# Performance work log

Measured on AMD Instinct MI355X. Metric: run time of the kernel, lower is better.

## Reference

```python
import jax, jax.numpy as jnp
import numpy as np

B, T_NEW, D_MODEL, H, DH = 8, 512, 1024, 16, 64
CACHED = 2048
T_TOTAL = CACHED + T_NEW  # static padded total length (last batch item is full)


def setup_inputs() -> dict:
    key = jax.random.key(0)
    ks = jax.random.split(key, 16)
    x_new = jax.random.normal(ks[0], (B, T_NEW, D_MODEL), jnp.float32)
    past_lengths = jax.random.randint(ks[1], (B,), CACHED // 2, CACHED)
    past_lengths = past_lengths.at[-1].set(CACHED).astype(jnp.int32)
    new_counts = jax.random.randint(ks[2], (B,), 1, T_NEW)
    new_counts = new_counts.at[-1].set(T_NEW).astype(jnp.int32)
    # prefix (left-aligned) valid mask for new tokens, matching how the torch
    # module compacts k_new[b, :, :count] into the cache
    valid_new_mask = jnp.arange(T_NEW)[None, :] < new_counts[:, None]
    total_lengths = past_lengths + new_counts
    key_padding_mask = jnp.arange(T_TOTAL)[None, :] < total_lengths[:, None]
    inv_freq = 1.0 / (10000.0 ** (jnp.arange(0, DH, 2, dtype=jnp.float32) / DH))
    pm = (jnp.arange(CACHED)[None, :] < past_lengths[:, None])[:, None, :, None]
    past_k = jax.random.normal(ks[3], (B, H, CACHED, DH), jnp.float32) * pm
    past_v = jax.random.normal(ks[4], (B, H, CACHED, DH), jnp.float32) * pm
    s = 0.02
    Wq = jax.random.normal(ks[5], (D_MODEL, D_MODEL), jnp.float32) * s
    Wk = jax.random.normal(ks[6], (D_MODEL, D_MODEL), jnp.float32) * s
    Wv = jax.random.normal(ks[7], (D_MODEL, D_MODEL), jnp.float32) * s
    Wo = jax.random.normal(ks[8], (D_MODEL, D_MODEL), jnp.float32) * s
    bq = jnp.zeros((D_MODEL,), jnp.float32)
    bk = jnp.zeros((D_MODEL,), jnp.float32)
    bv = jnp.zeros((D_MODEL,), jnp.float32)
    bo = jnp.zeros((D_MODEL,), jnp.float32)
    return {
        'x_new': x_new, 'inv_freq': inv_freq, 'past_k': past_k, 'past_v': past_v,
        'Wq': Wq, 'bq': bq, 'Wk': Wk, 'bk': bk, 'Wv': Wv, 'bv': bv, 'Wo': Wo, 'bo': bo,
        'key_padding_mask': key_padding_mask, 'past_lengths': past_lengths,
        'valid_new_mask': valid_new_mask,
    }


def _rotate_half(x):
    h = x.shape[-1] // 2
    return jnp.concatenate([-x[..., h:], x[..., :h]], axis=-1)


def reference(x_new, inv_freq, past_k, past_v, Wq, bq, Wk, bk, Wv, bv, Wo, bo,
              key_padding_mask, past_lengths, valid_new_mask):
    Bb, Tn, _ = x_new.shape
    # projections -> [B, H, T_new, DH]
    q = (x_new @ Wq.T + bq).reshape(Bb, Tn, H, DH).transpose(0, 2, 1, 3)
    k_new = (x_new @ Wk.T + bk).reshape(Bb, Tn, H, DH).transpose(0, 2, 1, 3)
    v_new = (x_new @ Wv.T + bv).reshape(Bb, Tn, H, DH).transpose(0, 2, 1, 3)
    # RoPE at absolute positions past_len + step (invalid -> 0)
    steps = jnp.arange(Tn)
    positions = jnp.where(valid_new_mask, past_lengths[:, None] + steps[None, :], 0)
    freqs = positions[..., None].astype(jnp.float32) * inv_freq  # [B, T, DH/2]
    emb = jnp.concatenate([freqs, freqs], axis=-1)
    cos = jnp.cos(emb)[:, None].astype(q.dtype)  # [B, 1, T, DH]
    sin = jnp.sin(emb)[:, None].astype(q.dtype)
    q = q * cos + _rotate_half(q) * sin
    k_new = k_new * cos + _rotate_half(k_new) * sin
    vm = valid_new_mask[:, None, :, None].astype(q.dtype)
    q = q * vm
    k_new = k_new * vm
    v_new = v_new * vm
    # zero cached entries past each item's cached length (matches padded cache)
    pm = (jnp.arange(CACHED)[None, :] < past_lengths[:, None])[:, None, :, None]
    past_k = past_k * pm.astype(past_k.dtype)
    past_v = past_v * pm.astype(past_v.dtype)
    # ragged append: scatter new tokens at [past_len, past_len+count); invalid
    # tokens dumped into an extra slot T_TOTAL that is sliced off
    pos_idx = jnp.where(valid_new_mask, past_lengths[:, None] + steps[None, :], T_TOTAL)
    pad = lambda p: jnp.pad(p, ((0, 0), (0, 0), (0, T_TOTAL + 1 - CACHED), (0, 0)))
    scat = jax.vmap(lambda base, new, idx: base.at[:, idx, :].add(new))
    k_total = scat(pad(past_k), k_new, pos_idx)[:, :, :T_TOTAL]
    v_total = scat(pad(past_v), v_new, pos_idx)[:, :, :T_TOTAL]
    # padded SDPA with key-padding mask
    scores = jnp.einsum('bhqd,bhkd->bhqk', q, k_total) / jnp.sqrt(jnp.asarray(DH, q.dtype))
    scores = jnp.where(key_padding_mask[:, None, None, :], scores, jnp.finfo(scores.dtype).min)
    attn = jax.nn.softmax(scores, axis=-1)
    ctx = jnp.einsum('bhqk,bhkd->bhqd', attn, v_total)
    ctx = ctx.transpose(0, 2, 1, 3).reshape(Bb, Tn, D_MODEL)
    out = (ctx @ Wo.T + bo) * valid_new_mask[..., None].astype(ctx.dtype)
    total_lengths = past_lengths + valid_new_mask.sum(axis=1).astype(past_lengths.dtype)
    return out, k_total, v_total, total_lengths
```

## Files before the change

kernel.cpp:

```cpp
#include <hip/hip_runtime.h>
#include <math.h>

#define B_ 8
#define TN 512
#define DM 1024
#define H_ 16
#define DH 64
#define CACHED_ 2048
#define TT 2560

#define QSC 0.18033688011112042f

typedef __attribute__((ext_vector_type(8))) short bf16x8;
typedef __attribute__((ext_vector_type(4))) float f32x4;

union U16x8 { uint4 u; unsigned short s[8]; };
union U16x4 { uint2 u; unsigned short s[4]; };
union F4 { float4 v; float f[4]; };

__device__ __forceinline__ unsigned short f2b(float x) {
    unsigned u = __float_as_uint(x);
    unsigned r = (u + 0x7FFFu + ((u >> 16) & 1u)) >> 16;
    return (unsigned short)r;
}
__device__ __forceinline__ float b2f(unsigned short v) {
    return __uint_as_float((unsigned)v << 16);
}

__device__ __forceinline__ unsigned cvt_pk_bf16(float lo, float hi) {
    unsigned r;
    asm("v_cvt_pk_bf16_f32 %0, %1, %2" : "=v"(r) : "v"(lo), "v"(hi));
    return r;
}

__device__ __forceinline__ void gload16(const void* g, void* l) {
    __builtin_amdgcn_global_load_lds(
        (const __attribute__((address_space(1))) void*)g,
        (__attribute__((address_space(3))) void*)l, 16, 0, 0);
}

__global__ void count_kernel(const unsigned char* __restrict__ vnm,
                             const unsigned char* __restrict__ kpm,
                             const int* __restrict__ past_len,
                             int* __restrict__ counts,
                             float* __restrict__ total_out) {
    int b = blockIdx.x;
    __shared__ int red[256];
    int esz = (kpm[1] | kpm[2] | kpm[3]) ? 1 : 4;
    int s = 0;
    for (int t = threadIdx.x; t < TN; t += 256)
        s += (vnm[(size_t)(b * TN + t) * esz] != 0) ? 1 : 0;
    red[threadIdx.x] = s;
    __syncthreads();
    for (int off = 128; off > 0; off >>= 1) {
        if (threadIdx.x < off) red[threadIdx.x] += red[threadIdx.x + off];
        __syncthreads();
    }
    if (threadIdx.x == 0) {
        counts[b] = red[0];
        total_out[b] = (float)(past_len[b] + red[0]);
    }
}

__global__ void cvt_all(const float* __restrict__ x,
                        const float* __restrict__ Wq,
                        const float* __restrict__ Wk,
                        const float* __restrict__ Wv,
                        const float* __restrict__ Wo,
                        unsigned short* __restrict__ Xbf,
                        unsigned short* __restrict__ Wqkvb,
                        unsigned short* __restrict__ Wob) {
    int i8 = (blockIdx.x * 256 + threadIdx.x) << 3;
    const float* src;
    unsigned short* dst;
    int off;
    if (i8 < (1 << 22)) {
        src = x; off = i8; dst = Xbf + i8;
    } else if (i8 < (1 << 22) + (3 << 20)) {
        int j = i8 - (1 << 22);
        int w = j >> 20;
        src = w == 0 ? Wq : (w == 1 ? Wk : Wv);
        off = j & 0xFFFFF;
        dst = Wqkvb + j;
    } else {
        int j = i8 - ((1 << 22) + (3 << 20));
        src = Wo; off = j; dst = Wob + j;
    }
    float4 a = *(const float4*)(src + off);
    float4 b = *(const float4*)(src + off + 4);
    U16x8 o;
    o.s[0] = f2b(a.x); o.s[1] = f2b(a.y); o.s[2] = f2b(a.z); o.s[3] = f2b(a.w);
    o.s[4] = f2b(b.x); o.s[5] = f2b(b.y); o.s[6] = f2b(b.z); o.s[7] = f2b(b.w);
    *(uint4*)dst = o.u;
}

__device__ __forceinline__ void gemm_core(
    const unsigned short* __restrict__ A, const unsigned short* __restrict__ Bw,
    int K, int m0, int n0, short* As, short* Bs, f32x4 acc[4][4]) {
    const int tid = threadIdx.x;
    const int wave = tid >> 6, lane = tid & 63;
    const int wm = wave >> 1, wn = wave & 1;
    const int l15 = lane & 15, lq = lane >> 4;

    const int srow = wave * 16 + (lane >> 2);
    const int sc = (lane & 3) << 3;
    const unsigned short* Ag0 = A + (size_t)(m0 + srow) * K + sc;
    const unsigned short* Ag1 = A + (size_t)(m0 + 64 + srow) * K + sc;
    const unsigned short* Bg0 = Bw + (size_t)(n0 + srow) * K + sc;
    const unsigned short* Bg1 = Bw + (size_t)(n0 + 64 + srow) * K + sc;
    short* Ad0 = As + wave * 16 * 32;
    short* Ad1 = As + (64 + wave * 16) * 32;
    short* Bd0 = Bs + wave * 16 * 32;
    short* Bd1 = Bs + (64 + wave * 16) * 32;

    for (int k0 = 0; k0 < K; k0 += 32) {
        __syncthreads();
        gload16(Ag0 + k0, Ad0);
        gload16(Ag1 + k0, Ad1);
        gload16(Bg0 + k0, Bd0);
        gload16(Bg1 + k0, Bd1);
        __syncthreads();
        bf16x8 af[4], bf[4];
#pragma unroll
        for (int mi = 0; mi < 4; ++mi)
            af[mi] = *(const bf16x8*)&As[(wm * 64 + mi * 16 + l15) * 32 + lq * 8];
#pragma unroll
        for (int ni = 0; ni < 4; ++ni)
            bf[ni] = *(const bf16x8*)&Bs[(wn * 64 + ni * 16 + l15) * 32 + lq * 8];
#pragma unroll
        for (int mi = 0; mi < 4; ++mi)
#pragma unroll
            for (int ni = 0; ni < 4; ++ni)
                acc[mi][ni] = __builtin_amdgcn_mfma_f32_16x16x32_bf16(
                    af[mi], bf[ni], acc[mi][ni], 0, 0, 0);
    }
}

__global__ __launch_bounds__(256) void gemm_qkv_mfma(
    const unsigned short* __restrict__ Xbf,
    const unsigned short* __restrict__ Wqkv,
    const float* __restrict__ bq, const float* __restrict__ bk,
    const float* __restrict__ bv, const float* __restrict__ inv_freq,
    const int* __restrict__ past_len,
    unsigned short* __restrict__ Qraw, unsigned short* __restrict__ Kraw,
    unsigned short* __restrict__ Vraw) {
    __shared__ __align__(16) short As[128 * 32];
    __shared__ __align__(16) short Bs[128 * 32];
    f32x4 acc[4][4] = {};
    const int m0 = blockIdx.y << 7, n0 = blockIdx.x << 7;
    gemm_core(Xbf, Wqkv, DM, m0, n0, As, Bs, acc);

    const int which = n0 >> 10;
    const int tid = threadIdx.x, wave = tid >> 6, lane = tid & 63;
    const int wm = wave >> 1, wn = wave & 1, l15 = lane & 15, lq = lane >> 4;

    if (which == 0) {
        const int bb = m0 >> 9;
        const int pl = past_len[bb];
        const int hh = (n0 + wn * 64) >> 6;
#pragma unroll
        for (int ni = 0; ni < 2; ++ni) {
            int i = ni * 16 + l15;
            int n1 = n0 + wn * 64 + ni * 16 + l15;
            float fi = inv_freq[i];
            float blo = bq[n1], bhi = bq[n1 + 32];
#pragma unroll
            for (int mi = 0; mi < 4; ++mi) {
#pragma unroll
                for (int r = 0; r < 4; ++r) {
                    int m = m0 + wm * 64 + mi * 16 + lq * 4 + r;
                    int t = m & 511;
                    float ang = (float)(pl + t) * fi;
                    float s, c;
                    __sincosf(ang, &s, &c);
                    float x1 = acc[mi][ni][r] + blo;
                    float x2 = acc[mi][ni + 2][r] + bhi;
                    size_t base = ((size_t)(bb * H_ + hh) * TN + t) * DH;
                    Qraw[base + i]      = f2b((x1 * c - x2 * s) * QSC);
                    Qraw[base + i + 32] = f2b((x2 * c + x1 * s) * QSC);
                }
            }
        }
    } else {
        const float* bias = which == 1 ? bk : bv;
        unsigned short* dst = which == 1 ? Kraw : Vraw;
#pragma unroll
        for (int ni = 0; ni < 4; ++ni) {
            int n1 = (n0 & 1023) + wn * 64 + ni * 16 + l15;
            float bb = bias[n1];
            int h = n1 >> 6, dh = n1 & 63;
#pragma unroll
            for (int mi = 0; mi < 4; ++mi) {
#pragma unroll
                for (int r = 0; r < 4; ++r) {
                    int m = m0 + wm * 64 + mi * 16 + lq * 4 + r;
                    int b = m >> 9, t = m & 511;
                    dst[((size_t)(b * H_ + h) * TN + t) * DH + dh] =
                        f2b(acc[mi][ni][r] + bb);
                }
            }
        }
    }
}

__global__ __launch_bounds__(256) void gemm_out_mfma(
    const unsigned short* __restrict__ Ctxb,
    const unsigned short* __restrict__ Wob,
    const float* __restrict__ bo, const int* __restrict__ counts,
    float* __restrict__ Out) {
    __shared__ __align__(16) short As[128 * 32];
    __shared__ __align__(16) short Bs[128 * 32];
    f32x4 acc[4][4] = {};
    const int m0 = blockIdx.y << 7, n0 = blockIdx.x << 7;
    gemm_core(Ctxb, Wob, DM, m0, n0, As, Bs, acc);

    const int tid = threadIdx.x, wave = tid >> 6, lane = tid & 63;
    const int wm = wave >> 1, wn = wave & 1, l15 = lane & 15, lq = lane >> 4;
    const int cnt = counts[m0 >> 9];
#pragma unroll
    for (int mi = 0; mi < 4; ++mi) {
#pragma unroll
        for (int r = 0; r < 4; ++r) {
            int m = m0 + wm * 64 + mi * 16 + lq * 4 + r;
            int t = m & 511;
            bool valid = t < cnt;
#pragma unroll
            for (int ni = 0; ni < 4; ++ni) {
                int n = n0 + wn * 64 + ni * 16 + l15;
                Out[(size_t)m * DM + n] = valid ? acc[mi][ni][r] + bo[n] : 0.f;
            }
        }
    }
}

__global__ void build_kv(const float* __restrict__ past_k,
                         const float* __restrict__ past_v,
                         const unsigned short* __restrict__ Kraw,
                         const unsigned short* __restrict__ Vraw,
                         const float* __restrict__ inv_freq,
                         const int* __restrict__ past_len,
                         const int* __restrict__ counts,
                         float* __restrict__ Ko, float* __restrict__ Vo,
                         unsigned short* __restrict__ Kb16,
                         unsigned short* __restrict__ Vb16) {
    int idx = blockIdx.x * 256 + threadIdx.x;
    int i = idx & 7;
    int p = idx >> 3;
    int h = blockIdx.y, bz = blockIdx.z;
    int pl = past_len[bz], cnt = counts[bz];
    int dh = i << 2;
    size_t obase = ((size_t)(bz * H_ + h) * TT + p) * DH;
    F4 k1, k2, v1, v2;
    if (p < pl) {
        size_t ib = ((size_t)(bz * H_ + h) * CACHED_ + p) * DH;
        k1.v = *(const float4*)(past_k + ib + dh);
        k2.v = *(const float4*)(past_k + ib + dh + 32);
        v1.v = *(const float4*)(past_v + ib + dh);
        v2.v = *(const float4*)(past_v + ib + dh + 32);
    } else if (p < pl + cnt) {
        int t = p - pl;
        size_t ib = ((size_t)(bz * H_ + h) * TN + t) * DH;
        U16x4 ka, kc, va, vc;
        ka.u = *(const uint2*)(Kraw + ib + dh);
        kc.u = *(const uint2*)(Kraw + ib + dh + 32);
        va.u = *(const uint2*)(Vraw + ib + dh);
        vc.u = *(const uint2*)(Vraw + ib + dh + 32);
#pragma unroll
        for (int j = 0; j < 4; ++j) {
            float ang = (float)p * inv_freq[dh + j];
            float s, c;
            __sincosf(ang, &s, &c);
            float x1 = b2f(ka.s[j]), x2 = b2f(kc.s[j]);
            k1.f[j] = x1 * c - x2 * s;
            k2.f[j] = x2 * c + x1 * s;
            v1.f[j] = b2f(va.s[j]);
            v2.f[j] = b2f(vc.s[j]);
        }
    } else {
        k1.v = k2.v = v1.v = v2.v = make_float4(0.f, 0.f, 0.f, 0.f);
    }
    *(float4*)(Ko + obase + dh) = k1.v;
    *(float4*)(Ko + obase + dh + 32) = k2.v;
    *(float4*)(Vo + obase + dh) = v1.v;
    *(float4*)(Vo + obase + dh + 32) = v2.v;
    U16x4 o;
#pragma unroll
    for (int j = 0; j < 4; ++j) o.s[j] = f2b(k1.f[j]);
    *(uint2*)(Kb16 + obase + dh) = o.u;
#pragma unroll
    for (int j = 0; j < 4; ++j) o.s[j] = f2b(k2.f[j]);
    *(uint2*)(Kb16 + obase + dh + 32) = o.u;
#pragma unroll
    for (int j = 0; j < 4; ++j) o.s[j] = f2b(v1.f[j]);
    *(uint2*)(Vb16 + obase + dh) = o.u;
#pragma unroll
    for (int j = 0; j < 4; ++j) o.s[j] = f2b(v2.f[j]);
    *(uint2*)(Vb16 + obase + dh + 32) = o.u;
}

__global__ __launch_bounds__(256) void attn_mfma(
    const unsigned short* __restrict__ Qbf,
    const unsigned short* __restrict__ Kb,
    const unsigned short* __restrict__ Vb,
    const int* __restrict__ past_len, const int* __restrict__ counts,
    unsigned short* __restrict__ Ctxb) {
    const int j = blockIdx.x;
    const int xcd = j & 7;
    const int tloc = j >> 3;
    const int qt = tloc & 7;
    const int p = ((tloc >> 3) << 3) | xcd;
    const int b = p >> 4, h = p & 15;

    const int tid = threadIdx.x;
    const int wave = tid >> 6, lane = tid & 63;
    const int l15 = lane & 15, lq = lane >> 4;

    __shared__ __align__(16) short Qs[4096];
    __shared__ __align__(16) short Ks[2][4096];
    __shared__ __align__(16) short Vt[4096];
    __shared__ __align__(16) short Pb[4096];

    const size_t qbase = ((size_t)(b * H_ + h) * TN + qt * 64) * DH;
    const size_t kbase = (size_t)(b * H_ + h) * TT * DH;

    const int total = past_len[b] + counts[b];
    const int ntiles = (total + 63) >> 6;

    const int dA = wave * 64 + lane;
    const int dB = 256 + wave * 64 + lane;
    const int krA = (dA >> 7) * 16 + ((dA & 15) ^ ((dA >> 4) & 7));
    const int kcA = ((dA >> 4) & 7) << 3;
    const int krB = (dB >> 7) * 16 + ((dB & 15) ^ ((dB >> 4) & 7));
    const int kcB = ((dB >> 4) & 7) << 3;
    const unsigned short* KgA = Kb + kbase + (size_t)krA * DH + kcA;
    const unsigned short* KgB = Kb + kbase + (size_t)krB * DH + kcB;
    const int kdoffA = (wave * 64) * 8;
    const int kdoffB = (256 + wave * 64) * 8;

    gload16(KgA, &Ks[0][kdoffA]);
    gload16(KgB, &Ks[0][kdoffB]);

    const int kp = tid & 31, dh8 = (tid >> 5) << 3;
    const int kc = kp >> 2, ko2 = (kp & 3) << 1;
    const unsigned short* Vg = Vb + kbase + (size_t)(2 * kp) * DH + dh8;
    uint4 vr0 = *(const uint4*)Vg;
    uint4 vr1 = *(const uint4*)(Vg + DH);

#pragma unroll
    for (int jj = 0; jj < 2; ++jj) {
        int e = tid + (jj << 8);
        int row = e >> 3, c = e & 7;
        *(uint4*)&Qs[(((row >> 4) * 8 + c) * 16 + ((row & 15) ^ c)) * 8] =
            *(const uint4*)(Qbf + qbase + row * 64 + c * 8);
    }
    __syncthreads();
    const int c0 = lq, c1 = 4 + lq;
    bf16x8 qa0 = *(const bf16x8*)&Qs[((wave * 8 + c0) * 16 + (l15 ^ c0)) * 8];
    bf16x8 qa1 = *(const bf16x8*)&Qs[((wave * 8 + c1) * 16 + (l15 ^ c1)) * 8];

    float rsum[4] = {0.f, 0.f, 0.f, 0.f};
    f32x4 O[4] = {};
    unsigned short* Pw = (unsigned short*)(Pb + wave * 1024);
    const int pc0 = l15 >> 3, pwo = l15 & 7;

    int cur = 0;
    for (int kt = 0; kt < ntiles; ++kt) {
        asm volatile("s_waitcnt vmcnt(0)" ::: "memory");
        __builtin_amdgcn_s_barrier();

        {
            U16x8 a, cc;
            a.u = vr0;
            cc.u = vr1;
#pragma unroll
            for (int jj = 0; jj < 8; ++jj) {
                int dh = dh8 + jj;
                unsigned pk = (unsigned)a.s[jj] | ((unsigned)cc.s[jj] << 16);
                *(unsigned*)&Vt[((((dh >> 4) * 8 + kc) * 16) + ((dh & 15) ^ kc)) * 8 + ko2] = pk;
            }
        }
        {
            int ktn = (kt + 1 < ntiles) ? kt + 1 : kt;
            gload16(KgA + (size_t)ktn * 64 * DH, &Ks[cur ^ 1][kdoffA]);
            gload16(KgB + (size_t)ktn * 64 * DH, &Ks[cur ^ 1][kdoffB]);
            vr0 = *(const uint4*)(Vg + (size_t)ktn * 64 * DH);
            vr1 = *(const uint4*)(Vg + (size_t)ktn * 64 * DH + DH);
        }

        asm volatile("s_waitcnt lgkmcnt(0)" ::: "memory");
        __builtin_amdgcn_s_barrier();
        __builtin_amdgcn_sched_barrier(0);

        const short* Kcur = Ks[cur];
        f32x4 S[4];
#pragma unroll
        for (int nt = 0; nt < 4; ++nt) {
            f32x4 acc = {};
            bf16x8 kb0 = *(const bf16x8*)&Kcur[((nt * 8 + c0) * 16 + (l15 ^ c0)) * 8];
            acc = __builtin_amdgcn_mfma_f32_16x16x32_bf16(qa0, kb0, acc, 0, 0, 0);
            bf16x8 kb1 = *(const bf16x8*)&Kcur[((nt * 8 + c1) * 16 + (l15 ^ c1)) * 8];
            acc = __builtin_amdgcn_mfma_f32_16x16x32_bf16(qa1, kb1, acc, 0, 0, 0);
            S[nt] = acc;
        }

        int limit = total - (kt << 6);
        if (limit < 64) {
#pragma unroll
            for (int nt = 0; nt < 4; ++nt) {
                bool ok = nt * 16 + l15 < limit;
#pragma unroll
                for (int r = 0; r < 4; ++r) S[nt][r] = ok ? S[nt][r] : -1e30f;
            }
        }

#pragma unroll
        for (int nt = 0; nt < 4; ++nt) {
            const int pc = nt * 2 + pc0;
#pragma unroll
            for (int rr = 0; rr < 2; ++rr) {
                float p0 = __builtin_amdgcn_exp2f(S[nt][2 * rr]);
                float p1 = __builtin_amdgcn_exp2f(S[nt][2 * rr + 1]);
                rsum[2 * rr] += p0;
                rsum[2 * rr + 1] += p1;
                unsigned pk = cvt_pk_bf16(p0, p1);
                int row0 = lq * 4 + 2 * rr;
                int row1 = row0 + 1;
                Pw[(pc * 16 + (row0 ^ pc)) * 8 + pwo] = (unsigned short)pk;
                Pw[(pc * 16 + (row1 ^ pc)) * 8 + pwo] = (unsigned short)(pk >> 16);
            }
        }
        asm volatile("s_waitcnt lgkmcnt(0)" ::: "memory");

        bf16x8 pa0 = *(const bf16x8*)&Pw[(c0 * 16 + (l15 ^ c0)) * 8];
        bf16x8 pa1 = *(const bf16x8*)&Pw[(c1 * 16 + (l15 ^ c1)) * 8];
#pragma unroll
        for (int nt = 0; nt < 4; ++nt) {
            bf16x8 vb0 = *(const bf16x8*)&Vt[((nt * 8 + c0) * 16 + (l15 ^ c0)) * 8];
            O[nt] = __builtin_amdgcn_mfma_f32_16x16x32_bf16(pa0, vb0, O[nt], 0, 0, 0);
            bf16x8 vb1 = *(const bf16x8*)&Vt[((nt * 8 + c1) * 16 + (l15 ^ c1)) * 8];
            O[nt] = __builtin_amdgcn_mfma_f32_16x16x32_bf16(pa1, vb1, O[nt], 0, 0, 0);
        }
        cur ^= 1;
    }

#pragma unroll
    for (int off = 1; off < 16; off <<= 1)
#pragma unroll
        for (int r = 0; r < 4; ++r) rsum[r] += __shfl_xor(rsum[r], off);

#pragma unroll
    for (int r = 0; r < 4; ++r) {
        float inv = 1.f / rsum[r];
        int t = qt * 64 + wave * 16 + lq * 4 + r;
        size_t mbase = ((size_t)(b * TN + t)) * DM + h * DH;
#pragma unroll
        for (int nt = 0; nt < 4; ++nt)
            Ctxb[mbase + nt * 16 + l15] = f2b(O[nt][r] * inv);
    }
}

extern "C" void kernel_launch(void* const* d_in, const int* in_sizes, int n_in,
                              void* d_out, int out_size, void* d_ws, size_t ws_size,
                              hipStream_t stream) {
    const float* x_new    = (const float*)d_in[0];
    const float* inv_freq = (const float*)d_in[1];
    const float* past_k   = (const float*)d_in[2];
    const float* past_v   = (const float*)d_in[3];
    const float* Wq = (const float*)d_in[4];
    const float* bq = (const float*)d_in[5];
    const float* Wk = (const float*)d_in[6];
    const float* bk = (const float*)d_in[7];
    const float* Wv = (const float*)d_in[8];
    const float* bv = (const float*)d_in[9];
    const float* Wo = (const float*)d_in[10];
    const float* bo = (const float*)d_in[11];
    const unsigned char* kpm = (const unsigned char*)d_in[12];
    const int* past_len      = (const int*)d_in[13];
    const unsigned char* vnm = (const unsigned char*)d_in[14];

    float* out      = (float*)d_out;
    float* k_total  = out + (size_t)B_ * TN * DM;
    float* v_total  = k_total + (size_t)B_ * H_ * TT * DH;
    float* total_out = v_total + (size_t)B_ * H_ * TT * DH;

    const size_t NQ = (size_t)B_ * TN * DM;
    const size_t NKV = (size_t)B_ * H_ * TT * DH;

    int* counts = (int*)d_ws;
    unsigned short* Xbf   = (unsigned short*)((char*)d_ws + 256);
    unsigned short* Wqkvb = Xbf + NQ;
    unsigned short* Wob   = Wqkvb + (size_t)3 * DM * DM;
    unsigned short* Qraw  = Wob + (size_t)DM * DM;
    unsigned short* Kraw  = Qraw + NQ;
    unsigned short* Vraw  = Kraw + NQ;
    unsigned short* Ctxb  = Vraw + NQ;
    unsigned short* Kb16  = Ctxb + NQ;
    unsigned short* Vb16  = Kb16 + NKV;

    count_kernel<<<B_, 256, 0, stream>>>(vnm, kpm, past_len, counts, total_out);
    cvt_all<<<4096, 256, 0, stream>>>(x_new, Wq, Wk, Wv, Wo, Xbf, Wqkvb, Wob);

    gemm_qkv_mfma<<<dim3(24, 32), 256, 0, stream>>>(
        Xbf, Wqkvb, bq, bk, bv, inv_freq, past_len, Qraw, Kraw, Vraw);
    build_kv<<<dim3((TT * 8) / 256, H_, B_), 256, 0, stream>>>(
        past_k, past_v, Kraw, Vraw, inv_freq, past_len, counts,
        k_total, v_total, Kb16, Vb16);
    attn_mfma<<<1024, 256, 0, stream>>>(Qraw, Kb16, Vb16,
                                        past_len, counts, Ctxb);
    gemm_out_mfma<<<dim3(8, 32), 256, 0, stream>>>(Ctxb, Wob, bo, counts, out);
}
```

Before: 527.1 us.

## Double-buffer GEMM LDS tiles and widen attention blocks to 128 queries

The shared GEMM core now double-buffers its A/B LDS tiles, prefetching the next K slice while MFMAs run on the current one, with one barrier per iteration instead of two. The attention kernel moves to 512-thread blocks covering 128 query rows, so each K/V tile loaded into LDS is reused by twice as many waves and the per-thread K/V load work is halved. The cost is more LDS per block, which can lower occupancy. The GEMM prefetch also relies on a single barrier plus a vmcnt wait for correctness.

```diff
diff --git a/kernel.cpp b/kernel.cpp
--- a/kernel.cpp
+++ b/kernel.cpp
@@ -96,7 +96,7 @@
 
 __device__ __forceinline__ void gemm_core(
     const unsigned short* __restrict__ A, const unsigned short* __restrict__ Bw,
-    int K, int m0, int n0, short* As, short* Bs, f32x4 acc[4][4]) {
+    int K, int m0, int n0, short* As2, short* Bs2, f32x4 acc[4][4]) {
     const int tid = threadIdx.x;
     const int wave = tid >> 6, lane = tid & 63;
     const int wm = wave >> 1, wn = wave & 1;
@@ -108,31 +108,43 @@
     const unsigned short* Ag1 = A + (size_t)(m0 + 64 + srow) * K + sc;
     const unsigned short* Bg0 = Bw + (size_t)(n0 + srow) * K + sc;
     const unsigned short* Bg1 = Bw + (size_t)(n0 + 64 + srow) * K + sc;
-    short* Ad0 = As + wave * 16 * 32;
-    short* Ad1 = As + (64 + wave * 16) * 32;
-    short* Bd0 = Bs + wave * 16 * 32;
-    short* Bd1 = Bs + (64 + wave * 16) * 32;
-
+    const int d0 = wave * 512;
+    const int d1 = 2048 + wave * 512;
+
+    gload16(Ag0, As2 + d0);
+    gload16(Ag1, As2 + d1);
+    gload16(Bg0, Bs2 + d0);
+    gload16(Bg1, Bs2 + d1);
+
+    int cur = 0;
     for (int k0 = 0; k0 < K; k0 += 32) {
-        __syncthreads();
-        gload16(Ag0 + k0, Ad0);
-        gload16(Ag1 + k0, Ad1);
-        gload16(Bg0 + k0, Bd0);
-        gload16(Bg1 + k0, Bd1);
-        __syncthreads();
+        asm volatile("s_waitcnt vmcnt(0)" ::: "memory");
+        __builtin_amdgcn_s_barrier();
+
+        int kn = (k0 + 32 < K) ? k0 + 32 : k0;
+        short* An = As2 + ((cur ^ 1) << 12);
+        short* Bn = Bs2 + ((cur ^ 1) << 12);
+        gload16(Ag0 + kn, An + d0);
+        gload16(Ag1 + kn, An + d1);
+        gload16(Bg0 + kn, Bn + d0);
+        gload16(Bg1 + kn, Bn + d1);
+
+        const short* Ac = As2 + (cur << 12);
+        const short* Bc = Bs2 + (cur << 12);
         bf16x8 af[4], bf[4];
 #pragma unroll
         for (int mi = 0; mi < 4; ++mi)
-            af[mi] = *(const bf16x8*)&As[(wm * 64 + mi * 16 + l15) * 32 + lq * 8];
+            af[mi] = *(const bf16x8*)&Ac[(wm * 64 + mi * 16 + l15) * 32 + lq * 8];
 #pragma unroll
         for (int ni = 0; ni < 4; ++ni)
-            bf[ni] = *(const bf16x8*)&Bs[(wn * 64 + ni * 16 + l15) * 32 + lq * 8];
+            bf[ni] = *(const bf16x8*)&Bc[(wn * 64 + ni * 16 + l15) * 32 + lq * 8];
 #pragma unroll
         for (int mi = 0; mi < 4; ++mi)
 #pragma unroll
             for (int ni = 0; ni < 4; ++ni)
                 acc[mi][ni] = __builtin_amdgcn_mfma_f32_16x16x32_bf16(
                     af[mi], bf[ni], acc[mi][ni], 0, 0, 0);
+        cur ^= 1;
     }
 }
 
@@ -144,8 +156,8 @@
     const int* __restrict__ past_len,
     unsigned short* __restrict__ Qraw, unsigned short* __restrict__ Kraw,
     unsigned short* __restrict__ Vraw) {
-    __shared__ __align__(16) short As[128 * 32];
-    __shared__ __align__(16) short Bs[128 * 32];
+    __shared__ __align__(16) short As[2 * 128 * 32];
+    __shared__ __align__(16) short Bs[2 * 128 * 32];
     f32x4 acc[4][4] = {};
     const int m0 = blockIdx.y << 7, n0 = blockIdx.x << 7;
     gemm_core(Xbf, Wqkv, DM, m0, n0, As, Bs, acc);
@@ -208,8 +220,8 @@
     const unsigned short* __restrict__ Wob,
     const float* __restrict__ bo, const int* __restrict__ counts,
     float* __restrict__ Out) {
-    __shared__ __align__(16) short As[128 * 32];
-    __shared__ __align__(16) short Bs[128 * 32];
+    __shared__ __align__(16) short As[2 * 128 * 32];
+    __shared__ __align__(16) short Bs[2 * 128 * 32];
     f32x4 acc[4][4] = {};
     const int m0 = blockIdx.y << 7, n0 = blockIdx.x << 7;
     gemm_core(Ctxb, Wob, DM, m0, n0, As, Bs, acc);
@@ -298,7 +310,7 @@
     *(uint2*)(Vb16 + obase + dh + 32) = o.u;
 }
 
-__global__ __launch_bounds__(256) void attn_mfma(
+__global__ __launch_bounds__(512) void attn_mfma(
     const unsigned short* __restrict__ Qbf,
     const unsigned short* __restrict__ Kb,
     const unsigned short* __restrict__ Vb,
@@ -307,48 +319,43 @@
     const int j = blockIdx.x;
     const int xcd = j & 7;
     const int tloc = j >> 3;
-    const int qt = tloc & 7;
-    const int p = ((tloc >> 3) << 3) | xcd;
+    const int qt = tloc & 3;
+    const int p = ((tloc >> 2) << 3) | xcd;
     const int b = p >> 4, h = p & 15;
 
     const int tid = threadIdx.x;
     const int wave = tid >> 6, lane = tid & 63;
     const int l15 = lane & 15, lq = lane >> 4;
 
-    __shared__ __align__(16) short Qs[4096];
+    __shared__ __align__(16) short Qs[8192];
     __shared__ __align__(16) short Ks[2][4096];
     __shared__ __align__(16) short Vt[4096];
-    __shared__ __align__(16) short Pb[4096];
-
-    const size_t qbase = ((size_t)(b * H_ + h) * TN + qt * 64) * DH;
+    __shared__ __align__(16) short Pb[8192];
+
+    const size_t qbase = ((size_t)(b * H_ + h) * TN + qt * 128) * DH;
     const size_t kbase = (size_t)(b * H_ + h) * TT * DH;
 
     const int total = past_len[b] + counts[b];
     const int ntiles = (total + 63) >> 6;
 
-    const int dA = wave * 64 + lane;
-    const int dB = 256 + wave * 64 + lane;
+    const int dA = tid;
     const int krA = (dA >> 7) * 16 + ((dA & 15) ^ ((dA >> 4) & 7));
     const int kcA = ((dA >> 4) & 7) << 3;
-    const int krB = (dB >> 7) * 16 + ((dB & 15) ^ ((dB >> 4) & 7));
-    const int kcB = ((dB >> 4) & 7) << 3;
     const unsigned short* KgA = Kb + kbase + (size_t)krA * DH + kcA;
-    const unsigned short* KgB = Kb + kbase + (size_t)krB * DH + kcB;
-    const int kdoffA = (wave * 64) * 8;
-    const int kdoffB = (256 + wave * 64) * 8;
+    const int kdoffA = wave * 512;
 
     gload16(KgA, &Ks[0][kdoffA]);
-    gload16(KgB, &Ks[0][kdoffB]);
-
-    const int kp = tid & 31, dh8 = (tid >> 5) << 3;
+
+    const int kp = tid & 31;
+    const int dh4 = (tid >> 5) << 2;
     const int kc = kp >> 2, ko2 = (kp & 3) << 1;
-    const unsigned short* Vg = Vb + kbase + (size_t)(2 * kp) * DH + dh8;
-    uint4 vr0 = *(const uint4*)Vg;
-    uint4 vr1 = *(const uint4*)(Vg + DH);
+    const unsigned short* Vg = Vb + kbase + (size_t)(2 * kp) * DH + dh4;
+    uint2 vr0 = *(const uint2*)Vg;
+    uint2 vr1 = *(const uint2*)(Vg + DH);
 
 #pragma unroll
     for (int jj = 0; jj < 2; ++jj) {
-        int e = tid + (jj << 8);
+        int e = tid + (jj << 9);
         int row = e >> 3, c = e & 7;
         *(uint4*)&Qs[(((row >> 4) * 8 + c) * 16 + ((row & 15) ^ c)) * 8] =
             *(const uint4*)(Qbf + qbase + row * 64 + c * 8);
@@ -369,12 +376,12 @@
         __builtin_amdgcn_s_barrier();
 
         {
-            U16x8 a, cc;
+            U16x4 a, cc;
             a.u = vr0;
             cc.u = vr1;
 #pragma unroll
-            for (int jj = 0; jj < 8; ++jj) {
-                int dh = dh8 + jj;
+            for (int jj = 0; jj < 4; ++jj) {
+                int dh = dh4 + jj;
                 unsigned pk = (unsigned)a.s[jj] | ((unsigned)cc.s[jj] << 16);
                 *(unsigned*)&Vt[((((dh >> 4) * 8 + kc) * 16) + ((dh & 15) ^ kc)) * 8 + ko2] = pk;
             }
@@ -382,9 +389,8 @@
         {
             int ktn = (kt + 1 < ntiles) ? kt + 1 : kt;
             gload16(KgA + (size_t)ktn * 64 * DH, &Ks[cur ^ 1][kdoffA]);
-            gload16(KgB + (size_t)ktn * 64 * DH, &Ks[cur ^ 1][kdoffB]);
-            vr0 = *(const uint4*)(Vg + (size_t)ktn * 64 * DH);
-            vr1 = *(const uint4*)(Vg + (size_t)ktn * 64 * DH + DH);
+            vr0 = *(const uint2*)(Vg + (size_t)ktn * 64 * DH);
+            vr1 = *(const uint2*)(Vg + (size_t)ktn * 64 * DH + DH);
         }
 
         asm volatile("s_waitcnt lgkmcnt(0)" ::: "memory");
@@ -451,7 +457,7 @@
 #pragma unroll
     for (int r = 0; r < 4; ++r) {
         float inv = 1.f / rsum[r];
-        int t = qt * 64 + wave * 16 + lq * 4 + r;
+        int t = qt * 128 + wave * 16 + lq * 4 + r;
         size_t mbase = ((size_t)(b * TN + t)) * DM + h * DH;
 #pragma unroll
         for (int nt = 0; nt < 4; ++nt)
@@ -505,7 +511,7 @@
     build_kv<<<dim3((TT * 8) / 256, H_, B_), 256, 0, stream>>>(
         past_k, past_v, Kraw, Vraw, inv_freq, past_len, counts,
         k_total, v_total, Kb16, Vb16);
-    attn_mfma<<<1024, 256, 0, stream>>>(Qraw, Kb16, Vb16,
-                                        past_len, counts, Ctxb);
+    attn_mfma<<<512, 512, 0, stream>>>(Qraw, Kb16, Vb16,
+                                       past_len, counts, Ctxb);
     gemm_out_mfma<<<dim3(8, 32), 256, 0, stream>>>(Ctxb, Wob, bo, counts, out);
 }
```

Measured after the change: 496.2 us. -5.9%, faster.
